# Optimization experiments

Measured on AMD Instinct MI355X. Metric: run time of the kernel, lower is better.

Reference implementation:

```python
import jax, jax.numpy as jnp
import numpy as np

VOCAB, D_MODEL, NHEAD, NLAYER, DIM_FF, MAX_LEN = 32000, 1024, 16, 6, 4096, 1024
B, L = 8, 1024
PAD_ID = 0
EPS = 1e-5


def _ln(x, g, b):
    m = x.mean(-1, keepdims=True)
    v = x.var(-1, keepdims=True)
    return (x - m) / jnp.sqrt(v + EPS) * g + b


def _mha(x, Wqkv, bqkv, Wo, bo, kpm):
    # x: [B,L,D]; Wqkv: [3D,D]; kpm: [B,L] bool (True = padded key)
    Bx, Lx, D = x.shape
    dh = D // NHEAD
    qkv = x @ Wqkv.T + bqkv                       # [B,L,3D]
    q, k, v = jnp.split(qkv, 3, axis=-1)
    sp = lambda t: t.reshape(Bx, Lx, NHEAD, dh).transpose(0, 2, 1, 3)  # [B,H,L,dh]
    q, k, v = sp(q), sp(k), sp(v)
    scores = jnp.einsum('bhqd,bhkd->bhqk', q, k) * (dh ** -0.5)
    scores = jnp.where(kpm[:, None, None, :], jnp.asarray(-1e9, scores.dtype), scores)
    attn = jax.nn.softmax(scores, axis=-1)        # explicit weights, as ForceWeightsMHA demands
    o = jnp.einsum('bhqk,bhkd->bhqd', attn, v)
    o = o.transpose(0, 2, 1, 3).reshape(Bx, Lx, D)
    return o @ Wo.T + bo


def setup_inputs() -> dict:
    key = jax.random.key(0)
    ks = jax.random.split(key, 20)
    s = 0.02
    n = lambda k, shp: (jax.random.normal(k, shp, dtype=jnp.float32) * s)
    inp = {
        'input_ids': jax.random.randint(ks[0], (B, L), 0, VOCAB, dtype=jnp.int64) if jax.config.jax_enable_x64 else jax.random.randint(ks[0], (B, L), 0, VOCAB).astype(jnp.int32),
        'tok_emb': n(ks[1], (VOCAB, D_MODEL)),
        'pos_emb': n(ks[2], (MAX_LEN, D_MODEL)),
        'Wqkv': n(ks[3], (NLAYER, 3 * D_MODEL, D_MODEL)),
        'bqkv': jnp.zeros((NLAYER, 3 * D_MODEL), jnp.float32),
        'Wo': n(ks[4], (NLAYER, D_MODEL, D_MODEL)),
        'bo': jnp.zeros((NLAYER, D_MODEL), jnp.float32),
        'ln1_g': jnp.ones((NLAYER, D_MODEL), jnp.float32),
        'ln1_b': jnp.zeros((NLAYER, D_MODEL), jnp.float32),
        'W1': n(ks[5], (NLAYER, DIM_FF, D_MODEL)),
        'b1': jnp.zeros((NLAYER, DIM_FF), jnp.float32),
        'W2': n(ks[6], (NLAYER, D_MODEL, DIM_FF)),
        'b2': jnp.zeros((NLAYER, D_MODEL), jnp.float32),
        'ln2_g': jnp.ones((NLAYER, D_MODEL), jnp.float32),
        'ln2_b': jnp.zeros((NLAYER, D_MODEL), jnp.float32),
        'head_ln_g': jnp.ones((D_MODEL,), jnp.float32),
        'head_ln_b': jnp.zeros((D_MODEL,), jnp.float32),
        'head_W': n(ks[7], (MAX_LEN, D_MODEL)),
        'head_b': jnp.zeros((MAX_LEN,), jnp.float32),
    }
    return inp


def reference(input_ids, tok_emb, pos_emb, Wqkv, bqkv, Wo, bo, ln1_g, ln1_b,
              W1, b1, W2, b2, ln2_g, ln2_b, head_ln_g, head_ln_b, head_W, head_b):
    Bx, Lx = input_ids.shape
    x = tok_emb[input_ids] + pos_emb[None, :Lx]           # [B,L,D]
    kpm = (input_ids == PAD_ID).at[:, 0].set(False)        # key padding mask, col 0 forced valid
    for i in range(NLAYER):                                # post-norm encoder layer (PyTorch default)
        x = _ln(x + _mha(x, Wqkv[i], bqkv[i], Wo[i], bo[i], kpm), ln1_g[i], ln1_b[i])
        ff = jax.nn.gelu(x @ W1[i].T + b1[i], approximate=False) @ W2[i].T + b2[i]
        x = _ln(x + ff, ln2_g[i], ln2_b[i])
    cls = x[:, 0, :]                                       # [B,D]
    return _ln(cls, head_ln_g, head_ln_b) @ head_W.T + head_b  # [B,MAX_LEN]
```

## Files before the change

kernel.cpp:

```cpp
#include <hip/hip_runtime.h>
#include <cstdint>

#define D_MODEL 1024
#define NHEAD   16
#define NLAYER  6
#define DIM_FF  4096
#define SEQ_B   8
#define SEQ_L   1024
#define TOKENS  (SEQ_B*SEQ_L)

typedef __bf16 v8bf  __attribute__((ext_vector_type(8)));
typedef __bf16 v4bf  __attribute__((ext_vector_type(4)));
typedef float  v4f   __attribute__((ext_vector_type(4)));

__device__ __forceinline__ void gl_lds16(const void* g, void* l) {
  __builtin_amdgcn_global_load_lds(
      (const __attribute__((address_space(1))) void*)g,
      (__attribute__((address_space(3))) void*)l, 16, 0, 0);
}

__global__ __launch_bounds__(256) void f2b_kernel(const float4* __restrict__ in,
                                                  ushort4* __restrict__ out, long n4) {
  long i = (long)blockIdx.x * 256 + threadIdx.x;
  long stride = (long)gridDim.x * 256;
  for (; i < n4; i += stride) {
    float4 v = in[i];
    v4bf r = { (__bf16)v.x, (__bf16)v.y, (__bf16)v.z, (__bf16)v.w };
    out[i] = *(ushort4*)&r;
  }
}

__global__ __launch_bounds__(256) void embed_kernel(const int* __restrict__ ids,
    const float4* __restrict__ tok, const float4* __restrict__ pos,
    float4* __restrict__ X, ushort4* __restrict__ Xb) {
  long i = (long)blockIdx.x * 256 + threadIdx.x;
  int d4 = (int)(i & 255);
  long bl = i >> 8;
  int l = (int)(bl & (SEQ_L - 1));
  int id = ids[bl];
  float4 t = tok[(long)id * 256 + d4];
  float4 p = pos[(long)l * 256 + d4];
  float4 v = {t.x + p.x, t.y + p.y, t.z + p.z, t.w + p.w};
  X[i] = v;
  v4bf r = { (__bf16)v.x, (__bf16)v.y, (__bf16)v.z, (__bf16)v.w };
  Xb[i] = *(ushort4*)&r;
}

__global__ __launch_bounds__(256) void maskb_kernel(const int* __restrict__ ids,
                                                    float* __restrict__ mb) {
  int i = blockIdx.x * 256 + threadIdx.x;
  mb[i] = (ids[i] == 0 && (i & 1023) != 0) ? -1e9f : 0.f;
}

#define MM16(AF, BF, FO) \
  { _Pragma("unroll") for (int f_ = 0; f_ < 4; ++f_) { \
      _Pragma("unroll") for (int j_ = 0; j_ < 4; ++j_) \
        acc[(FO)+f_][j_] = __builtin_amdgcn_mfma_f32_16x16x32_bf16(AF[f_], BF[j_], acc[(FO)+f_][j_], 0, 0, 0); } }
#define MM8(AF, BF, FO) \
  { _Pragma("unroll") for (int f_ = 0; f_ < 4; ++f_) { \
      _Pragma("unroll") for (int j_ = 0; j_ < 2; ++j_) \
        acc[(FO)+f_][j_] = __builtin_amdgcn_mfma_f32_16x16x32_bf16(AF[f_], BF[j_], acc[(FO)+f_][j_], 0, 0, 0); } }

#define STA(c,h,kt) { const unsigned short* s_ = pA + (long)(m0 + (h)*128)*K + ((long)(kt)<<6); \
  gl_lds16(s_,                 dAs + (c)*16384 + (h)*8192); \
  gl_lds16(s_ + ((long)K<<6),  dAs + (c)*16384 + (h)*8192 + 4096); }
#define STB(c,h,kt) { const unsigned short* s_ = pW + (long)(n0 + (h)*128)*K + ((long)(kt)<<6); \
  gl_lds16(s_,                 dBs + (c)*16384 + (h)*8192); \
  gl_lds16(s_ + ((long)K<<6),  dBs + (c)*16384 + (h)*8192 + 4096); }
#define STB2(c,kt) { const unsigned short* s_ = pW + (long)n0*K + ((long)(kt)<<6); \
  gl_lds16(s_,                 dBs + (c)*8192); \
  gl_lds16(s_ + ((long)K<<6),  dBs + (c)*8192 + 4096); }

#define LGKM0  asm volatile("s_waitcnt lgkmcnt(0)" ::: "memory")
#define VMCNT4 asm volatile("s_waitcnt vmcnt(4)" ::: "memory")
#define BARR   __builtin_amdgcn_s_barrier()
#define SCHED0 __builtin_amdgcn_sched_barrier(0)

template<int EPI>
__global__ __launch_bounds__(512, 2) void gemm256(
    const unsigned short* __restrict__ A,
    const unsigned short* __restrict__ W,
    const float* __restrict__ bias,
    unsigned short* __restrict__ Cb,
    unsigned short* __restrict__ Vt,
    int M, int N, int K) {
  __shared__ unsigned short As[2][16384];
  __shared__ unsigned short Bs[2][16384];
  int tid = threadIdx.x;
  int wave = tid >> 6, lane = tid & 63;
  int l15 = lane & 15, quad = lane >> 4;
  int wm = wave >> 2;
  int wn = wave & 3;

  int id = blockIdx.y * gridDim.x + blockIdx.x;
  int xcd = id & 7, sidx = id >> 3;
  int mt = xcd * 4 + (sidx & 3);
  int nt = sidx >> 2;
  int m0 = mt * 256, n0 = nt * 256;

  int srow = tid >> 3;
  int scol = ((tid & 7) ^ ((tid >> 4) & 7)) << 3;
  const unsigned short* pA = A + (long)srow * K + scol;
  const unsigned short* pW = W + (long)srow * K + scol;
  unsigned short* dAs = &As[0][0] + (tid << 3);
  unsigned short* dBs = &Bs[0][0] + (tid << 3);

  int offA[8], offB[4];
  #pragma unroll
  for (int f = 0; f < 8; ++f) {
    int r = wm * 128 + f * 16 + l15;
    offA[f] = r * 64 + ((quad ^ ((r >> 1) & 7)) << 3);
  }
  #pragma unroll
  for (int j = 0; j < 4; ++j) {
    int r = wn * 64 + j * 16 + l15;
    offB[j] = r * 64 + ((quad ^ ((r >> 1) & 7)) << 3);
  }

  v4f acc[8][4];
  #pragma unroll
  for (int f = 0; f < 8; ++f)
    #pragma unroll
    for (int j = 0; j < 4; ++j) acc[f][j] = (v4f){0.f, 0.f, 0.f, 0.f};

  int KT = K >> 6;
  STA(0, 0, 0); STA(0, 1, 0); STB(0, 0, 0); STB(0, 1, 0);
  STA(1, 0, 1); STA(1, 1, 1);
  VMCNT4; BARR; SCHED0;

  const unsigned short* as0 = &As[0][0];
  const unsigned short* bs0 = &Bs[0][0];
  const unsigned short* as1 = &As[1][0];
  const unsigned short* bs1 = &Bs[1][0];

  for (int tb = 0; tb < KT; tb += 2) {
    int kt2 = (tb + 2 < KT) ? tb + 2 : KT - 1;
    int kt3 = (tb + 3 < KT) ? tb + 3 : KT - 1;
    v8bf aA[4], aB[4], aC[4], aD[4], bA[4], bB[4];
    #pragma unroll
    for (int f = 0; f < 4; ++f) aA[f] = *(const v8bf*)(as0 + offA[f]);
    #pragma unroll
    for (int j = 0; j < 4; ++j) bA[j] = *(const v8bf*)(bs0 + offB[j]);
    #pragma unroll
    for (int j = 0; j < 4; ++j) bB[j] = *(const v8bf*)(bs0 + (offB[j] ^ 32));
    STB(1, 0, tb + 1);
    __builtin_amdgcn_s_setprio(1); MM16(aA, bA, 0); __builtin_amdgcn_s_setprio(0);
    #pragma unroll
    for (int f = 0; f < 4; ++f) aB[f] = *(const v8bf*)(as0 + (offA[f] ^ 32));
    STB(1, 1, tb + 1);
    __builtin_amdgcn_s_setprio(1); MM16(aB, bB, 0); __builtin_amdgcn_s_setprio(0);
    LGKM0; BARR; SCHED0;
    #pragma unroll
    for (int f = 0; f < 4; ++f) aC[f] = *(const v8bf*)(as0 + offA[4 + f]);
    #pragma unroll
    for (int f = 0; f < 4; ++f) aD[f] = *(const v8bf*)(as0 + (offA[4 + f] ^ 32));
    STB(0, 0, kt2);
    __builtin_amdgcn_s_setprio(1); MM16(aC, bA, 4); __builtin_amdgcn_s_setprio(0);
    STB(0, 1, kt2);
    __builtin_amdgcn_s_setprio(1); MM16(aD, bB, 4); __builtin_amdgcn_s_setprio(0);
    LGKM0; VMCNT4; BARR; SCHED0;
    #pragma unroll
    for (int f = 0; f < 4; ++f) aA[f] = *(const v8bf*)(as1 + offA[f]);
    #pragma unroll
    for (int j = 0; j < 4; ++j) bA[j] = *(const v8bf*)(bs1 + offB[j]);
    #pragma unroll
    for (int j = 0; j < 4; ++j) bB[j] = *(const v8bf*)(bs1 + (offB[j] ^ 32));
    STA(0, 0, kt2);
    __builtin_amdgcn_s_setprio(1); MM16(aA, bA, 0); __builtin_amdgcn_s_setprio(0);
    #pragma unroll
    for (int f = 0; f < 4; ++f) aB[f] = *(const v8bf*)(as1 + (offA[f] ^ 32));
    #pragma unroll
    for (int f = 0; f < 4; ++f) aC[f] = *(const v8bf*)(as1 + offA[4 + f]);
    #pragma unroll
    for (int f = 0; f < 4; ++f) aD[f] = *(const v8bf*)(as1 + (offA[4 + f] ^ 32));
    STA(0, 1, kt2);
    __builtin_amdgcn_s_setprio(1); MM16(aB, bB, 0); __builtin_amdgcn_s_setprio(0);
    LGKM0; BARR; SCHED0;
    STA(1, 0, kt3);
    __builtin_amdgcn_s_setprio(1); MM16(aC, bA, 4); __builtin_amdgcn_s_setprio(0);
    STA(1, 1, kt3);
    __builtin_amdgcn_s_setprio(1); MM16(aD, bB, 4); __builtin_amdgcn_s_setprio(0);
    VMCNT4; BARR; SCHED0;
  }

  #pragma unroll
  for (int f = 0; f < 8; ++f) {
    int crow0 = m0 + wm * 128 + f * 16 + quad * 4;
    #pragma unroll
    for (int j = 0; j < 4; ++j) {
      int col = n0 + wn * 64 + j * 16 + l15;
      float bv = bias[col];
      if (EPI == 3 && col >= 2048) {
        int hc = (col - 2048) >> 6, d = (col - 2048) & 63;
        int bb = crow0 >> 10, l = crow0 & 1023;
        v4bf pk = { (__bf16)(acc[f][j][0] + bv), (__bf16)(acc[f][j][1] + bv),
                    (__bf16)(acc[f][j][2] + bv), (__bf16)(acc[f][j][3] + bv) };
        *(ushort4*)&Vt[((long)((bb * 16 + hc) * 64 + d)) * 1024 + l] = *(ushort4*)&pk;
      } else {
        #pragma unroll
        for (int r = 0; r < 4; ++r) {
          float v = acc[f][j][r] + bv;
          if (EPI == 1) v = 0.5f * v * (1.f + erff(v * 0.70710678118f));
          ((__bf16*)Cb)[(long)(crow0 + r) * N + col] = (__bf16)v;
        }
      }
    }
  }
}

__global__ __launch_bounds__(512, 2) void gemm256n(
    const unsigned short* __restrict__ A,
    const unsigned short* __restrict__ W,
    const float* __restrict__ bias,
    float* __restrict__ Cf,
    int M, int N, int K) {
  __shared__ unsigned short As[2][16384];
  __shared__ unsigned short Bs[2][8192];
  int tid = threadIdx.x;
  int wave = tid >> 6, lane = tid & 63;
  int l15 = lane & 15, quad = lane >> 4;
  int wm = wave >> 2;
  int wn = wave & 3;

  int id = blockIdx.y * gridDim.x + blockIdx.x;
  int xcd = id & 7, sidx = id >> 3;
  int mt = xcd * 4 + (sidx & 3);
  int nt = sidx >> 2;
  int m0 = mt * 256, n0 = nt * 128;

  int srow = tid >> 3;
  int scol = ((tid & 7) ^ ((tid >> 4) & 7)) << 3;
  const unsigned short* pA = A + (long)srow * K + scol;
  const unsigned short* pW = W + (long)srow * K + scol;
  unsigned short* dAs = &As[0][0] + (tid << 3);
  unsigned short* dBs = &Bs[0][0] + (tid << 3);

  int offA[8], offB[2];
  #pragma unroll
  for (int f = 0; f < 8; ++f) {
    int r = wm * 128 + f * 16 + l15;
    offA[f] = r * 64 + ((quad ^ ((r >> 1) & 7)) << 3);
  }
  #pragma unroll
  for (int j = 0; j < 2; ++j) {
    int r = wn * 32 + j * 16 + l15;
    offB[j] = r * 64 + ((quad ^ ((r >> 1) & 7)) << 3);
  }

  v4f acc[8][2];
  #pragma unroll
  for (int f = 0; f < 8; ++f)
    #pragma unroll
    for (int j = 0; j < 2; ++j) acc[f][j] = (v4f){0.f, 0.f, 0.f, 0.f};

  int KT = K >> 6;
  STA(0, 0, 0); STA(0, 1, 0); STB2(0, 0);
  STA(1, 0, 1); STA(1, 1, 1);
  VMCNT4; BARR; SCHED0;

  const unsigned short* as0 = &As[0][0];
  const unsigned short* bs0 = &Bs[0][0];
  const unsigned short* as1 = &As[1][0];
  const unsigned short* bs1 = &Bs[1][0];

  for (int tb = 0; tb < KT; tb += 2) {
    int kt2 = (tb + 2 < KT) ? tb + 2 : KT - 1;
    int kt3 = (tb + 3 < KT) ? tb + 3 : KT - 1;
    v8bf aA[4], aB[4], aC[4], aD[4], bA[2], bB[2];
    #pragma unroll
    for (int f = 0; f < 4; ++f) aA[f] = *(const v8bf*)(as0 + offA[f]);
    #pragma unroll
    for (int j = 0; j < 2; ++j) bA[j] = *(const v8bf*)(bs0 + offB[j]);
    #pragma unroll
    for (int j = 0; j < 2; ++j) bB[j] = *(const v8bf*)(bs0 + (offB[j] ^ 32));
    STB2(1, tb + 1);
    __builtin_amdgcn_s_setprio(1); MM8(aA, bA, 0); __builtin_amdgcn_s_setprio(0);
    #pragma unroll
    for (int f = 0; f < 4; ++f) aB[f] = *(const v8bf*)(as0 + (offA[f] ^ 32));
    #pragma unroll
    for (int f = 0; f < 4; ++f) aC[f] = *(const v8bf*)(as0 + offA[4 + f]);
    #pragma unroll
    for (int f = 0; f < 4; ++f) aD[f] = *(const v8bf*)(as0 + (offA[4 + f] ^ 32));
    __builtin_amdgcn_s_setprio(1); MM8(aB, bB, 0); __builtin_amdgcn_s_setprio(0);
    LGKM0; BARR; SCHED0;
    STA(0, 0, kt2);
    __builtin_amdgcn_s_setprio(1); MM8(aC, bA, 4); __builtin_amdgcn_s_setprio(0);
    STA(0, 1, kt2);
    __builtin_amdgcn_s_setprio(1); MM8(aD, bB, 4); __builtin_amdgcn_s_setprio(0);
    VMCNT4; BARR; SCHED0;
    #pragma unroll
    for (int f = 0; f < 4; ++f) aA[f] = *(const v8bf*)(as1 + offA[f]);
    #pragma unroll
    for (int j = 0; j < 2; ++j) bA[j] = *(const v8bf*)(bs1 + offB[j]);
    #pragma unroll
    for (int j = 0; j < 2; ++j) bB[j] = *(const v8bf*)(bs1 + (offB[j] ^ 32));
    STB2(0, kt2);
    __builtin_amdgcn_s_setprio(1); MM8(aA, bA, 0); __builtin_amdgcn_s_setprio(0);
    #pragma unroll
    for (int f = 0; f < 4; ++f) aB[f] = *(const v8bf*)(as1 + (offA[f] ^ 32));
    #pragma unroll
    for (int f = 0; f < 4; ++f) aC[f] = *(const v8bf*)(as1 + offA[4 + f]);
    #pragma unroll
    for (int f = 0; f < 4; ++f) aD[f] = *(const v8bf*)(as1 + (offA[4 + f] ^ 32));
    __builtin_amdgcn_s_setprio(1); MM8(aB, bB, 0); __builtin_amdgcn_s_setprio(0);
    LGKM0; BARR; SCHED0;
    STA(1, 0, kt3);
    __builtin_amdgcn_s_setprio(1); MM8(aC, bA, 4); __builtin_amdgcn_s_setprio(0);
    STA(1, 1, kt3);
    __builtin_amdgcn_s_setprio(1); MM8(aD, bB, 4); __builtin_amdgcn_s_setprio(0);
    VMCNT4; BARR; SCHED0;
  }

  #pragma unroll
  for (int f = 0; f < 8; ++f) {
    int crow0 = m0 + wm * 128 + f * 16 + quad * 4;
    #pragma unroll
    for (int j = 0; j < 2; ++j) {
      int col = n0 + wn * 32 + j * 16 + l15;
      float bv = bias[col];
      #pragma unroll
      for (int r = 0; r < 4; ++r)
        Cf[(long)(crow0 + r) * N + col] = acc[f][j][r] + bv;
    }
  }
}

#define PSP 72
__global__ __launch_bounds__(256) void attn2(
    const unsigned short* __restrict__ QKVb,
    const unsigned short* __restrict__ Vtg,
    const float* __restrict__ mb,
    unsigned short* __restrict__ Ob) {
  __shared__ unsigned short Ks[64 * 64];
  __shared__ unsigned short Vs[64 * 64];
  __shared__ unsigned short Ps[4][16 * PSP];
  int tid = threadIdx.x, wave = tid >> 6, lane = tid & 63;
  int l15 = lane & 15, quad = lane >> 4;
  int b = blockIdx.z, h = blockIdx.y, q0 = blockIdx.x * 64;

  int qrow = q0 + wave * 16 + l15;
  const unsigned short* qb = QKVb + (long)(b * 1024 + qrow) * 3072 + h * 64;
  v8bf gq0 = *(const v8bf*)(qb + quad * 8);
  v8bf gq1 = *(const v8bf*)(qb + 32 + quad * 8);

  v8bf bones;
  #pragma unroll
  for (int j = 0; j < 8; ++j) bones[j] = (l15 == 0) ? (__bf16)1.0f : (__bf16)0.0f;

  float m_run[4], l_run[4];
  v4f O[4];
  #pragma unroll
  for (int r = 0; r < 4; ++r) { m_run[r] = -1e30f; l_run[r] = 0.f; }
  #pragma unroll
  for (int j = 0; j < 4; ++j) O[j] = (v4f){0.f, 0.f, 0.f, 0.f};

  const unsigned short* kgb = QKVb + (long)b * 1024 * 3072 + 1024 + h * 64;
  const unsigned short* vgb = Vtg + (long)((b * 16 + h) * 64) * 1024;
  const float* mrow = mb + b * 1024;

  int srow = tid >> 3;
  int ssl  = (tid & 7) ^ (srow & 7);
  int ph0 = (quad ^ (l15 & 7)) << 3;
  int ph1 = ((quad + 4) ^ (l15 & 7)) << 3;
  const float SC = 0.18033688011112042f;

  for (int k0 = 0; k0 < SEQ_L; k0 += 64) {
    __syncthreads();
    gl_lds16(kgb + (long)(k0 + srow) * 3072 + ssl * 8, &Ks[tid * 8]);
    gl_lds16(kgb + (long)(k0 + srow + 32) * 3072 + ssl * 8, &Ks[tid * 8 + 2048]);
    gl_lds16(vgb + (long)srow * 1024 + k0 + ssl * 8, &Vs[tid * 8]);
    gl_lds16(vgb + (long)(srow + 32) * 1024 + k0 + ssl * 8, &Vs[tid * 8 + 2048]);
    __syncthreads();

    float p[4][4], mr[4];
    #pragma unroll
    for (int r = 0; r < 4; ++r) mr[r] = -1e30f;
    #pragma unroll
    for (int t = 0; t < 4; ++t) {
      int kr = t * 16 + l15;
      v8bf kf0 = *(const v8bf*)&Ks[kr * 64 + ph0];
      v8bf kf1 = *(const v8bf*)&Ks[kr * 64 + ph1];
      v4f s = (v4f){0.f, 0.f, 0.f, 0.f};
      s = __builtin_amdgcn_mfma_f32_16x16x32_bf16(gq0, kf0, s, 0, 0, 0);
      s = __builtin_amdgcn_mfma_f32_16x16x32_bf16(gq1, kf1, s, 0, 0, 0);
      float bv = mrow[k0 + kr];
      #pragma unroll
      for (int r = 0; r < 4; ++r) {
        float sv = fmaf(s[r], SC, bv);
        p[t][r] = sv;
        mr[r] = fmaxf(mr[r], sv);
      }
    }
    #pragma unroll
    for (int r = 0; r < 4; ++r) {
      mr[r] = fmaxf(mr[r], __shfl_xor(mr[r], 1, 64));
      mr[r] = fmaxf(mr[r], __shfl_xor(mr[r], 2, 64));
      mr[r] = fmaxf(mr[r], __shfl_xor(mr[r], 4, 64));
      mr[r] = fmaxf(mr[r], __shfl_xor(mr[r], 8, 64));
    }
    float alpha[4];
    #pragma unroll
    for (int r = 0; r < 4; ++r) {
      float mn = fmaxf(m_run[r], mr[r]);
      alpha[r] = __builtin_amdgcn_exp2f(m_run[r] - mn);
      m_run[r] = mn;
    }
    #pragma unroll
    for (int t = 0; t < 4; ++t)
      #pragma unroll
      for (int r = 0; r < 4; ++r)
        p[t][r] = __builtin_amdgcn_exp2f(p[t][r] - m_run[r]);

    #pragma unroll
    for (int t = 0; t < 4; ++t)
      #pragma unroll
      for (int r = 0; r < 4; ++r)
        ((__bf16*)Ps[wave])[(quad * 4 + r) * PSP + t * 16 + l15] = (__bf16)p[t][r];
    v8bf pa0 = *(const v8bf*)&Ps[wave][l15 * PSP + quad * 8];
    v8bf pa1 = *(const v8bf*)&Ps[wave][l15 * PSP + 32 + quad * 8];

    v4f ss = (v4f){0.f, 0.f, 0.f, 0.f};
    ss = __builtin_amdgcn_mfma_f32_16x16x32_bf16(pa0, bones, ss, 0, 0, 0);
    ss = __builtin_amdgcn_mfma_f32_16x16x32_bf16(pa1, bones, ss, 0, 0, 0);

    #pragma unroll
    for (int j = 0; j < 4; ++j)
      #pragma unroll
      for (int r = 0; r < 4; ++r) O[j][r] *= alpha[r];
    #pragma unroll
    for (int j = 0; j < 4; ++j) {
      v8bf vf0 = *(const v8bf*)&Vs[(j * 16 + l15) * 64 + ph0];
      v8bf vf1 = *(const v8bf*)&Vs[(j * 16 + l15) * 64 + ph1];
      O[j] = __builtin_amdgcn_mfma_f32_16x16x32_bf16(pa0, vf0, O[j], 0, 0, 0);
      O[j] = __builtin_amdgcn_mfma_f32_16x16x32_bf16(pa1, vf1, O[j], 0, 0, 0);
    }
    #pragma unroll
    for (int r = 0; r < 4; ++r)
      l_run[r] = l_run[r] * alpha[r] + __shfl(ss[r], quad << 4, 64);
  }

  int qd = q0 + wave * 16 + quad * 4;
  #pragma unroll
  for (int r = 0; r < 4; ++r) {
    float inv = 1.f / l_run[r];
    #pragma unroll
    for (int j = 0; j < 4; ++j)
      ((__bf16*)Ob)[(long)(b * 1024 + qd + r) * 1024 + h * 64 + j * 16 + l15] =
          (__bf16)(O[j][r] * inv);
  }
}

__global__ __launch_bounds__(256) void add_ln(
    const float* __restrict__ Xin, const float* __restrict__ Yin,
    const float* __restrict__ g, const float* __restrict__ bta,
    float* __restrict__ outF, unsigned short* __restrict__ outB,
    long in_stride, long out_stride) {
  int row = blockIdx.x;
  const float* x = Xin + (long)row * in_stride;
  const float* y = Yin ? Yin + (long)row * 1024 : nullptr;
  int tid = threadIdx.x;
  float v[4];
  float s = 0.f, s2 = 0.f;
  #pragma unroll
  for (int j = 0; j < 4; ++j) {
    int d = j * 256 + tid;
    float t = x[d] + (y ? y[d] : 0.f);
    v[j] = t; s += t; s2 += t * t;
  }
  __shared__ float red[8];
  int lane = tid & 63, wave = tid >> 6;
  #pragma unroll
  for (int o = 32; o > 0; o >>= 1) { s += __shfl_down(s, o, 64); s2 += __shfl_down(s2, o, 64); }
  if (lane == 0) { red[wave] = s; red[4 + wave] = s2; }
  __syncthreads();
  s  = red[0] + red[1] + red[2] + red[3];
  s2 = red[4] + red[5] + red[6] + red[7];
  float mean = s * (1.f / 1024.f);
  float var  = s2 * (1.f / 1024.f) - mean * mean;
  float rstd = rsqrtf(var + 1e-5f);
  float* of = outF + (long)row * out_stride;
  unsigned short* ob = outB ? outB + (long)row * out_stride : nullptr;
  #pragma unroll
  for (int j = 0; j < 4; ++j) {
    int d = j * 256 + tid;
    float o = (v[j] - mean) * rstd * g[d] + bta[d];
    of[d] = o;
    if (ob) ((__bf16*)ob)[d] = (__bf16)o;
  }
}

__global__ __launch_bounds__(256) void head_kernel(
    const float* __restrict__ cls, const float* __restrict__ hW,
    const float* __restrict__ hb, float* __restrict__ out) {
  int n = blockIdx.x * 256 + threadIdx.x;
  int b = blockIdx.y;
  const float4* c4 = (const float4*)(cls + b * 1024);
  const float4* w4 = (const float4*)(hW + (long)n * 1024);
  float s = 0.f;
  #pragma unroll 8
  for (int d = 0; d < 256; ++d) {
    float4 a = c4[d], w = w4[d];
    s += a.x * w.x + a.y * w.y + a.z * w.z + a.w * w.w;
  }
  out[b * 1024 + n] = s + hb[n];
}

extern "C" void kernel_launch(void* const* d_in, const int* in_sizes, int n_in,
                              void* d_out, int out_size, void* d_ws, size_t ws_size,
                              hipStream_t stream) {
  const int*   ids  = (const int*)d_in[0];
  const float* tok  = (const float*)d_in[1];
  const float* pos  = (const float*)d_in[2];
  const float* Wqkv = (const float*)d_in[3];
  const float* bqkv = (const float*)d_in[4];
  const float* Wo   = (const float*)d_in[5];
  const float* bo   = (const float*)d_in[6];
  const float* ln1g = (const float*)d_in[7];
  const float* ln1b = (const float*)d_in[8];
  const float* W1   = (const float*)d_in[9];
  const float* b1   = (const float*)d_in[10];
  const float* W2   = (const float*)d_in[11];
  const float* b2   = (const float*)d_in[12];
  const float* ln2g = (const float*)d_in[13];
  const float* ln2b = (const float*)d_in[14];
  const float* hlng = (const float*)d_in[15];
  const float* hlnb = (const float*)d_in[16];
  const float* hW   = (const float*)d_in[17];
  const float* hb   = (const float*)d_in[18];
  float* out = (float*)d_out;

  char* ws = (char*)d_ws;
  size_t off = 0;
  auto alloc = [&](size_t bytes) {
    char* p = ws + off;
    off = (off + bytes + 255) & ~(size_t)255;
    return p;
  };
  unsigned short* Wqkv_b = (unsigned short*)alloc((size_t)NLAYER*3072*1024*2);
  unsigned short* Wo_b   = (unsigned short*)alloc((size_t)NLAYER*1024*1024*2);
  unsigned short* W1_b   = (unsigned short*)alloc((size_t)NLAYER*4096*1024*2);
  unsigned short* W2_b   = (unsigned short*)alloc((size_t)NLAYER*1024*4096*2);
  float*          X      = (float*)alloc((size_t)TOKENS*1024*4);
  unsigned short* Xb     = (unsigned short*)alloc((size_t)TOKENS*1024*2);
  unsigned short* Qb     = (unsigned short*)alloc((size_t)TOKENS*3072*2);
  unsigned short* Vtg    = (unsigned short*)alloc((size_t)TOKENS*1024*2);
  float*          Y      = (float*)alloc((size_t)TOKENS*1024*4);
  unsigned short* Ab     = (unsigned short*)alloc((size_t)TOKENS*1024*2);
  unsigned short* Gb     = Qb;
  float*          cls    = (float*)alloc(8*1024*4);
  float*          mb     = (float*)alloc(TOKENS*4);

  f2b_kernel<<<2048, 256, 0, stream>>>((const float4*)Wqkv, (ushort4*)Wqkv_b, (long)NLAYER*3072*1024/4);
  f2b_kernel<<<2048, 256, 0, stream>>>((const float4*)Wo,   (ushort4*)Wo_b,   (long)NLAYER*1024*1024/4);
  f2b_kernel<<<2048, 256, 0, stream>>>((const float4*)W1,   (ushort4*)W1_b,   (long)NLAYER*4096*1024/4);
  f2b_kernel<<<2048, 256, 0, stream>>>((const float4*)W2,   (ushort4*)W2_b,   (long)NLAYER*1024*4096/4);
  embed_kernel<<<(TOKENS*256)/256, 256, 0, stream>>>(ids, (const float4*)tok, (const float4*)pos,
                                                     (float4*)X, (ushort4*)Xb);
  maskb_kernel<<<TOKENS/256, 256, 0, stream>>>(ids, mb);

  for (int i = 0; i < NLAYER; ++i) {
    gemm256<3><<<dim3(3072/256, TOKENS/256), 512, 0, stream>>>(
        Xb, Wqkv_b + (size_t)i*3072*1024, bqkv + i*3072, Qb, Vtg, TOKENS, 3072, 1024);
    attn2<<<dim3(SEQ_L/64, NHEAD, SEQ_B), 256, 0, stream>>>(Qb, Vtg, mb, Ab);
    gemm256n<<<dim3(1024/128, TOKENS/256), 512, 0, stream>>>(
        Ab, Wo_b + (size_t)i*1024*1024, bo + i*1024, Y, TOKENS, 1024, 1024);
    add_ln<<<TOKENS, 256, 0, stream>>>(X, Y, ln1g + i*1024, ln1b + i*1024, X, Xb, 1024L, 1024L);
    gemm256<1><<<dim3(4096/256, TOKENS/256), 512, 0, stream>>>(
        Xb, W1_b + (size_t)i*4096*1024, b1 + i*4096, Gb, nullptr, TOKENS, 4096, 1024);
    gemm256n<<<dim3(1024/128, TOKENS/256), 512, 0, stream>>>(
        Gb, W2_b + (size_t)i*1024*4096, b2 + i*1024, Y, TOKENS, 1024, 4096);
    add_ln<<<TOKENS, 256, 0, stream>>>(X, Y, ln2g + i*1024, ln2b + i*1024, X, Xb, 1024L, 1024L);
  }
  add_ln<<<8, 256, 0, stream>>>(X, nullptr, hlng, hlnb, cls, nullptr, (long)SEQ_L*1024, 1024L);
  head_kernel<<<dim3(4, 8), 256, 0, stream>>>(cls, hW, hb, out);
}
```

Baseline: 2.879 ms.

## Restructure GEMM pipeline to prefetch A and B two tiles ahead; fast GELU

Reworks the double-buffered GEMM main loops so that each K-tile loads A and B for the tile two steps ahead into the buffer just consumed. This replaces the staggered scheme where B was loaded only one tile ahead, and it uses a deeper vmcnt wait so more global loads stay in flight with fewer barriers per tile. It also replaces erff in the GELU epilogue with an Abramowitz-Stegun polynomial using rcp and exp, which is cheaper but slightly less accurate.

```diff
diff --git a/kernel.cpp b/kernel.cpp
--- a/kernel.cpp
+++ b/kernel.cpp
@@ -17,6 +17,16 @@
   __builtin_amdgcn_global_load_lds(
       (const __attribute__((address_space(1))) void*)g,
       (__attribute__((address_space(3))) void*)l, 16, 0, 0);
+}
+
+__device__ __forceinline__ float gelu_f(float x) {
+  float z = fabsf(x) * 0.70710678118f;
+  float t = __builtin_amdgcn_rcpf(1.f + 0.3275911f * z);
+  float p = t * (0.254829592f + t * (-0.284496736f +
+            t * (1.421413741f + t * (-1.453152027f + t * 1.061405429f))));
+  float e = __expf(-z * z);
+  float erfz = 1.f - p * e;
+  return 0.5f * x * (1.f + copysignf(erfz, x));
 }
 
 __global__ __launch_bounds__(256) void f2b_kernel(const float4* __restrict__ in,
@@ -72,9 +82,46 @@
   gl_lds16(s_ + ((long)K<<6),  dBs + (c)*8192 + 4096); }
 
 #define LGKM0  asm volatile("s_waitcnt lgkmcnt(0)" ::: "memory")
-#define VMCNT4 asm volatile("s_waitcnt vmcnt(4)" ::: "memory")
+#define VMCNT6 asm volatile("s_waitcnt vmcnt(6)" ::: "memory")
+#define VMCNT8 asm volatile("s_waitcnt vmcnt(8)" ::: "memory")
 #define BARR   __builtin_amdgcn_s_barrier()
 #define SCHED0 __builtin_amdgcn_sched_barrier(0)
+
+#define GTILE(asP, bsP, c, ktn) { \
+    v8bf aA[4], aB[4], aC[4], aD[4], bA[4], bB[4]; \
+    _Pragma("unroll") for (int f = 0; f < 4; ++f) aA[f] = *(const v8bf*)(asP + offA[f]); \
+    _Pragma("unroll") for (int j = 0; j < 4; ++j) bA[j] = *(const v8bf*)(bsP + offB[j]); \
+    _Pragma("unroll") for (int j = 0; j < 4; ++j) bB[j] = *(const v8bf*)(bsP + (offB[j] ^ 32)); \
+    __builtin_amdgcn_s_setprio(1); MM16(aA, bA, 0); __builtin_amdgcn_s_setprio(0); \
+    _Pragma("unroll") for (int f = 0; f < 4; ++f) aB[f] = *(const v8bf*)(asP + (offA[f] ^ 32)); \
+    _Pragma("unroll") for (int f = 0; f < 4; ++f) aC[f] = *(const v8bf*)(asP + offA[4 + f]); \
+    _Pragma("unroll") for (int f = 0; f < 4; ++f) aD[f] = *(const v8bf*)(asP + (offA[4 + f] ^ 32)); \
+    __builtin_amdgcn_s_setprio(1); MM16(aB, bB, 0); __builtin_amdgcn_s_setprio(0); \
+    LGKM0; BARR; SCHED0; \
+    STA(c, 0, ktn); STB(c, 0, ktn); \
+    __builtin_amdgcn_s_setprio(1); MM16(aC, bA, 4); __builtin_amdgcn_s_setprio(0); \
+    STA(c, 1, ktn); STB(c, 1, ktn); \
+    __builtin_amdgcn_s_setprio(1); MM16(aD, bB, 4); __builtin_amdgcn_s_setprio(0); \
+    VMCNT8; BARR; SCHED0; \
+  }
+
+#define NTILE(asP, bsP, c, ktn) { \
+    v8bf aA[4], aB[4], aC[4], aD[4], bA[2], bB[2]; \
+    _Pragma("unroll") for (int f = 0; f < 4; ++f) aA[f] = *(const v8bf*)(asP + offA[f]); \
+    _Pragma("unroll") for (int j = 0; j < 2; ++j) bA[j] = *(const v8bf*)(bsP + offB[j]); \
+    _Pragma("unroll") for (int j = 0; j < 2; ++j) bB[j] = *(const v8bf*)(bsP + (offB[j] ^ 32)); \
+    __builtin_amdgcn_s_setprio(1); MM8(aA, bA, 0); __builtin_amdgcn_s_setprio(0); \
+    _Pragma("unroll") for (int f = 0; f < 4; ++f) aB[f] = *(const v8bf*)(asP + (offA[f] ^ 32)); \
+    _Pragma("unroll") for (int f = 0; f < 4; ++f) aC[f] = *(const v8bf*)(asP + offA[4 + f]); \
+    _Pragma("unroll") for (int f = 0; f < 4; ++f) aD[f] = *(const v8bf*)(asP + (offA[4 + f] ^ 32)); \
+    __builtin_amdgcn_s_setprio(1); MM8(aB, bB, 0); __builtin_amdgcn_s_setprio(0); \
+    LGKM0; BARR; SCHED0; \
+    STA(c, 0, ktn); STB2(c, ktn); \
+    __builtin_amdgcn_s_setprio(1); MM8(aC, bA, 4); __builtin_amdgcn_s_setprio(0); \
+    STA(c, 1, ktn); \
+    __builtin_amdgcn_s_setprio(1); MM8(aD, bB, 4); __builtin_amdgcn_s_setprio(0); \
+    VMCNT6; BARR; SCHED0; \
+  }
 
 template<int EPI>
 __global__ __launch_bounds__(512, 2) void gemm256(
@@ -124,9 +171,9 @@
     for (int j = 0; j < 4; ++j) acc[f][j] = (v4f){0.f, 0.f, 0.f, 0.f};
 
   int KT = K >> 6;
-  STA(0, 0, 0); STA(0, 1, 0); STB(0, 0, 0); STB(0, 1, 0);
-  STA(1, 0, 1); STA(1, 1, 1);
-  VMCNT4; BARR; SCHED0;
+  STA(0, 0, 0); STB(0, 0, 0); STA(0, 1, 0); STB(0, 1, 0);
+  STA(1, 0, 1); STB(1, 0, 1); STA(1, 1, 1); STB(1, 1, 1);
+  VMCNT8; BARR; SCHED0;
 
   const unsigned short* as0 = &As[0][0];
   const unsigned short* bs0 = &Bs[0][0];
@@ -136,51 +183,8 @@
   for (int tb = 0; tb < KT; tb += 2) {
     int kt2 = (tb + 2 < KT) ? tb + 2 : KT - 1;
     int kt3 = (tb + 3 < KT) ? tb + 3 : KT - 1;
-    v8bf aA[4], aB[4], aC[4], aD[4], bA[4], bB[4];
-    #pragma unroll
-    for (int f = 0; f < 4; ++f) aA[f] = *(const v8bf*)(as0 + offA[f]);
-    #pragma unroll
-    for (int j = 0; j < 4; ++j) bA[j] = *(const v8bf*)(bs0 + offB[j]);
-    #pragma unroll
-    for (int j = 0; j < 4; ++j) bB[j] = *(const v8bf*)(bs0 + (offB[j] ^ 32));
-    STB(1, 0, tb + 1);
-    __builtin_amdgcn_s_setprio(1); MM16(aA, bA, 0); __builtin_amdgcn_s_setprio(0);
-    #pragma unroll
-    for (int f = 0; f < 4; ++f) aB[f] = *(const v8bf*)(as0 + (offA[f] ^ 32));
-    STB(1, 1, tb + 1);
-    __builtin_amdgcn_s_setprio(1); MM16(aB, bB, 0); __builtin_amdgcn_s_setprio(0);
-    LGKM0; BARR; SCHED0;
-    #pragma unroll
-    for (int f = 0; f < 4; ++f) aC[f] = *(const v8bf*)(as0 + offA[4 + f]);
-    #pragma unroll
-    for (int f = 0; f < 4; ++f) aD[f] = *(const v8bf*)(as0 + (offA[4 + f] ^ 32));
-    STB(0, 0, kt2);
-    __builtin_amdgcn_s_setprio(1); MM16(aC, bA, 4); __builtin_amdgcn_s_setprio(0);
-    STB(0, 1, kt2);
-    __builtin_amdgcn_s_setprio(1); MM16(aD, bB, 4); __builtin_amdgcn_s_setprio(0);
-    LGKM0; VMCNT4; BARR; SCHED0;
-    #pragma unroll
-    for (int f = 0; f < 4; ++f) aA[f] = *(const v8bf*)(as1 + offA[f]);
-    #pragma unroll
-    for (int j = 0; j < 4; ++j) bA[j] = *(const v8bf*)(bs1 + offB[j]);
-    #pragma unroll
-    for (int j = 0; j < 4; ++j) bB[j] = *(const v8bf*)(bs1 + (offB[j] ^ 32));
-    STA(0, 0, kt2);
-    __builtin_amdgcn_s_setprio(1); MM16(aA, bA, 0); __builtin_amdgcn_s_setprio(0);
-    #pragma unroll
-    for (int f = 0; f < 4; ++f) aB[f] = *(const v8bf*)(as1 + (offA[f] ^ 32));
-    #pragma unroll
-    for (int f = 0; f < 4; ++f) aC[f] = *(const v8bf*)(as1 + offA[4 + f]);
-    #pragma unroll
-    for (int f = 0; f < 4; ++f) aD[f] = *(const v8bf*)(as1 + (offA[4 + f] ^ 32));
-    STA(0, 1, kt2);
-    __builtin_amdgcn_s_setprio(1); MM16(aB, bB, 0); __builtin_amdgcn_s_setprio(0);
-    LGKM0; BARR; SCHED0;
-    STA(1, 0, kt3);
-    __builtin_amdgcn_s_setprio(1); MM16(aC, bA, 4); __builtin_amdgcn_s_setprio(0);
-    STA(1, 1, kt3);
-    __builtin_amdgcn_s_setprio(1); MM16(aD, bB, 4); __builtin_amdgcn_s_setprio(0);
-    VMCNT4; BARR; SCHED0;
+    GTILE(as0, bs0, 0, kt2);
+    GTILE(as1, bs1, 1, kt3);
   }
 
   #pragma unroll
@@ -200,7 +204,7 @@
         #pragma unroll
         for (int r = 0; r < 4; ++r) {
           float v = acc[f][j][r] + bv;
-          if (EPI == 1) v = 0.5f * v * (1.f + erff(v * 0.70710678118f));
+          if (EPI == 1) v = gelu_f(v);
           ((__bf16*)Cb)[(long)(crow0 + r) * N + col] = (__bf16)v;
         }
       }
@@ -254,9 +258,9 @@
     for (int j = 0; j < 2; ++j) acc[f][j] = (v4f){0.f, 0.f, 0.f, 0.f};
 
   int KT = K >> 6;
-  STA(0, 0, 0); STA(0, 1, 0); STB2(0, 0);
-  STA(1, 0, 1); STA(1, 1, 1);
-  VMCNT4; BARR; SCHED0;
+  STA(0, 0, 0); STB2(0, 0); STA(0, 1, 0);
+  STA(1, 0, 1); STB2(1, 1); STA(1, 1, 1);
+  VMCNT6; BARR; SCHED0;
 
   const unsigned short* as0 = &As[0][0];
   const unsigned short* bs0 = &Bs[0][0];
@@ -266,49 +270,8 @@
   for (int tb = 0; tb < KT; tb += 2) {
     int kt2 = (tb + 2 < KT) ? tb + 2 : KT - 1;
     int kt3 = (tb + 3 < KT) ? tb + 3 : KT - 1;
-    v8bf aA[4], aB[4], aC[4], aD[4], bA[2], bB[2];
-    #pragma unroll
-    for (int f = 0; f < 4; ++f) aA[f] = *(const v8bf*)(as0 + offA[f]);
-    #pragma unroll
-    for (int j = 0; j < 2; ++j) bA[j] = *(const v8bf*)(bs0 + offB[j]);
-    #pragma unroll
-    for (int j = 0; j < 2; ++j) bB[j] = *(const v8bf*)(bs0 + (offB[j] ^ 32));
-    STB2(1, tb + 1);
-    __builtin_amdgcn_s_setprio(1); MM8(aA, bA, 0); __builtin_amdgcn_s_setprio(0);
-    #pragma unroll
-    for (int f = 0; f < 4; ++f) aB[f] = *(const v8bf*)(as0 + (offA[f] ^ 32));
-    #pragma unroll
-    for (int f = 0; f < 4; ++f) aC[f] = *(const v8bf*)(as0 + offA[4 + f]);
-    #pragma unroll
-    for (int f = 0; f < 4; ++f) aD[f] = *(const v8bf*)(as0 + (offA[4 + f] ^ 32));
-    __builtin_amdgcn_s_setprio(1); MM8(aB, bB, 0); __builtin_amdgcn_s_setprio(0);
-    LGKM0; BARR; SCHED0;
-    STA(0, 0, kt2);
-    __builtin_amdgcn_s_setprio(1); MM8(aC, bA, 4); __builtin_amdgcn_s_setprio(0);
-    STA(0, 1, kt2);
-    __builtin_amdgcn_s_setprio(1); MM8(aD, bB, 4); __builtin_amdgcn_s_setprio(0);
-    VMCNT4; BARR; SCHED0;
-    #pragma unroll
-    for (int f = 0; f < 4; ++f) aA[f] = *(const v8bf*)(as1 + offA[f]);
-    #pragma unroll
-    for (int j = 0; j < 2; ++j) bA[j] = *(const v8bf*)(bs1 + offB[j]);
-    #pragma unroll
-    for (int j = 0; j < 2; ++j) bB[j] = *(const v8bf*)(bs1 + (offB[j] ^ 32));
-    STB2(0, kt2);
-    __builtin_amdgcn_s_setprio(1); MM8(aA, bA, 0); __builtin_amdgcn_s_setprio(0);
-    #pragma unroll
-    for (int f = 0; f < 4; ++f) aB[f] = *(const v8bf*)(as1 + (offA[f] ^ 32));
-    #pragma unroll
-    for (int f = 0; f < 4; ++f) aC[f] = *(const v8bf*)(as1 + offA[4 + f]);
-    #pragma unroll
-    for (int f = 0; f < 4; ++f) aD[f] = *(const v8bf*)(as1 + (offA[4 + f] ^ 32));
-    __builtin_amdgcn_s_setprio(1); MM8(aB, bB, 0); __builtin_amdgcn_s_setprio(0);
-    LGKM0; BARR; SCHED0;
-    STA(1, 0, kt3);
-    __builtin_amdgcn_s_setprio(1); MM8(aC, bA, 4); __builtin_amdgcn_s_setprio(0);
-    STA(1, 1, kt3);
-    __builtin_amdgcn_s_setprio(1); MM8(aD, bB, 4); __builtin_amdgcn_s_setprio(0);
-    VMCNT4; BARR; SCHED0;
+    NTILE(as0, bs0, 0, kt2);
+    NTILE(as1, bs1, 1, kt3);
   }
 
   #pragma unroll
```

Result: faster. 2.781 ms (-3.4%).
